# Kernel tuning notes

Measured on AMD Instinct MI355X. Metric: run time of the kernel, lower is better.

The kernel has to match this reference:

```python
import jax, jax.numpy as jnp
import numpy as np


def _gcn_conv(x, W, b, src, dst, n_nodes):
    # PyG GCNConv with add_self_loops=True, edge_weight=None (implicit ones),
    # symmetric normalization: D^{-1/2} A_hat D^{-1/2} (X W) + b
    xw = x @ W                                    # [N, H]
    loop = jnp.arange(n_nodes, dtype=src.dtype)
    src_f = jnp.concatenate([src, loop])          # [E+N]
    dst_f = jnp.concatenate([dst, loop])          # [E+N]
    w = jnp.ones(src_f.shape[0], dtype=x.dtype)
    deg = jax.ops.segment_sum(w, dst_f, num_segments=n_nodes)  # in-degree incl. self-loop
    dinv = jnp.where(deg > 0, jax.lax.rsqrt(deg), 0.0)
    norm = dinv[src_f] * dinv[dst_f]              # [E+N]
    msgs = norm[:, None] * xw[src_f]              # [E+N, H]
    out = jax.ops.segment_sum(msgs, dst_f, num_segments=n_nodes)
    return out + b


def setup_inputs() -> dict:
    key = jax.random.key(0)
    k1, k2, k3, k4 = jax.random.split(key, 4)
    N, E, D, H = 100000, 1600000, 256, 128
    x = jax.random.normal(k1, (N, D), dtype=jnp.float32)
    edge_index = jax.random.randint(k2, (2, E), 0, N, dtype=jnp.int64)
    # Glorot-scaled weights
    W1 = jax.random.normal(k3, (D, H), dtype=jnp.float32) * np.sqrt(2.0 / (D + H))
    b1 = jnp.zeros((H,), dtype=jnp.float32)
    W2 = jax.random.normal(k4, (H, 1), dtype=jnp.float32) * np.sqrt(2.0 / (H + 1))
    b2 = jnp.zeros((1,), dtype=jnp.float32)
    return {"x": x, "edge_index": edge_index, "W1": W1, "b1": b1, "W2": W2, "b2": b2}


def reference(x, edge_index, W1, b1, W2, b2):
    n_nodes = x.shape[0]
    src, dst = edge_index[0], edge_index[1]
    h = _gcn_conv(x, W1, b1, src, dst, n_nodes)   # conv1
    h = jax.nn.relu(h)                            # relu; dropout is identity in eval mode
    out = _gcn_conv(h, W2, b2, src, dst, n_nodes) # conv2 -> [N, 1]
    return out.reshape(-1)                        # x.view(-1)
```

## Files before the change

kernel.cpp:

```cpp
#include <hip/hip_runtime.h>
#include <hip/hip_fp16.h>
#include <cstdint>
#include <cstddef>


#define BSH 9
#define BNODES (1 << BSH)
#define BPAD 16
#define BCAP 9216

typedef _Float16 half8 __attribute__((ext_vector_type(8)));
typedef float floatx4 __attribute__((ext_vector_type(4)));
typedef float floatv4 __attribute__((ext_vector_type(4)));
typedef int intv4 __attribute__((ext_vector_type(4)));
typedef unsigned int uintv4 __attribute__((ext_vector_type(4)));
typedef unsigned int uintv2 __attribute__((ext_vector_type(2)));

#define QK 0x64646464u
#define SEL01 0x00050004u
#define SEL23 0x00070006u

__device__ __forceinline__ void fmamix8(float (&acc)[8], uintv4 v, float w) {
  asm("v_fma_mix_f32 %0, %1, %2, %0 op_sel:[0,0,0] op_sel_hi:[0,1,0]"
      : "+v"(acc[0]) : "v"(w), "v"(v.x));
  asm("v_fma_mix_f32 %0, %1, %2, %0 op_sel:[0,1,0] op_sel_hi:[0,1,0]"
      : "+v"(acc[1]) : "v"(w), "v"(v.x));
  asm("v_fma_mix_f32 %0, %1, %2, %0 op_sel:[0,0,0] op_sel_hi:[0,1,0]"
      : "+v"(acc[2]) : "v"(w), "v"(v.y));
  asm("v_fma_mix_f32 %0, %1, %2, %0 op_sel:[0,1,0] op_sel_hi:[0,1,0]"
      : "+v"(acc[3]) : "v"(w), "v"(v.y));
  asm("v_fma_mix_f32 %0, %1, %2, %0 op_sel:[0,0,0] op_sel_hi:[0,1,0]"
      : "+v"(acc[4]) : "v"(w), "v"(v.z));
  asm("v_fma_mix_f32 %0, %1, %2, %0 op_sel:[0,1,0] op_sel_hi:[0,1,0]"
      : "+v"(acc[5]) : "v"(w), "v"(v.z));
  asm("v_fma_mix_f32 %0, %1, %2, %0 op_sel:[0,0,0] op_sel_hi:[0,1,0]"
      : "+v"(acc[6]) : "v"(w), "v"(v.w));
  asm("v_fma_mix_f32 %0, %1, %2, %0 op_sel:[0,1,0] op_sel_hi:[0,1,0]"
      : "+v"(acc[7]) : "v"(w), "v"(v.w));
}

__device__ __forceinline__ void fmaq8(float (&acc)[8], uintv2 q, float w) {
  uintv4 hw;
  hw.x = __builtin_amdgcn_perm(q.x, QK, SEL01);
  hw.y = __builtin_amdgcn_perm(q.x, QK, SEL23);
  hw.z = __builtin_amdgcn_perm(q.y, QK, SEL01);
  hw.w = __builtin_amdgcn_perm(q.y, QK, SEL23);
  fmamix8(acc, hw, w);
}

#define SWZF(v, imm) \
  __int_as_float(__builtin_amdgcn_ds_swizzle(__float_as_int(v), imm))

__global__ __launch_bounds__(256) void prep_k(const float* __restrict__ W1,
                                              _Float16* __restrict__ wz,
                                              unsigned char* __restrict__ z1q8,
                                              float* __restrict__ scp,
                                              float* __restrict__ z2w,
                                              int* __restrict__ cnt,
                                              int* __restrict__ gcur,
                                              int N, int NB) {
  int b = blockIdx.x, tid = threadIdx.x;
  if (b < 128) {
    int id = b * 256 + tid;
    int j = id & 7, lane = (id >> 3) & 63, nb = (id >> 9) & 7, kb = id >> 12;
    int k = kb * 32 + ((lane >> 4) << 3) + j;
    int n = nb * 16 + (lane & 15);
    wz[id] = (_Float16)W1[k * 128 + n];
  } else if (b == 128) {
    if (tid < 32) ((unsigned*)(z1q8 + (size_t)N * 128))[tid] = 0x80808080u;
    if (tid == 0) { z2w[N] = 0.f; cnt[N] = 1; scp[N] = 1.f; }
  } else {
    int i = (b - 129) * 256 + tid;
    if (i < NB * BPAD) gcur[i] = 0;
  }
}

template <int KIND>
__global__ __launch_bounds__(256) void stage_k(int fb, int g0,
                                               const float* __restrict__ X,
                                               const _Float16* __restrict__ wz,
                                               unsigned char* __restrict__ z1q8,
                                               float* __restrict__ scp, int N,
                                               const int* __restrict__ src,
                                               const int* __restrict__ dst,
                                               int* __restrict__ gcur,
                                               int* __restrict__ barr,
                                               int* __restrict__ ell,
                                               int* __restrict__ ell2,
                                               int* __restrict__ cnt,
                                               int E, int NB) {
  __shared__ char lds_raw[16 * 1024 + 256];
  int tid = threadIdx.x;

  if ((int)blockIdx.x < fb) {
    if (KIND == 0) {
      int* bc = (int*)lds_raw;
      int* bb = bc + 512;
      for (int i = tid; i < NB; i += 256) bc[i] = 0;
      __syncthreads();
      int base = ((int)blockIdx.x * 256 + tid) * 16;
      int dv[16], sv[16], rv[16], bkv[16];
      int ne = 0;
      if (base + 15 < E) {
#pragma unroll
        for (int q4 = 0; q4 < 4; ++q4) {
          intv4 d4 = __builtin_nontemporal_load((const intv4*)(dst + base + q4 * 4));
          intv4 s4 = __builtin_nontemporal_load((const intv4*)(src + base + q4 * 4));
          dv[q4 * 4 + 0] = d4[0]; dv[q4 * 4 + 1] = d4[1];
          dv[q4 * 4 + 2] = d4[2]; dv[q4 * 4 + 3] = d4[3];
          sv[q4 * 4 + 0] = s4[0]; sv[q4 * 4 + 1] = s4[1];
          sv[q4 * 4 + 2] = s4[2]; sv[q4 * 4 + 3] = s4[3];
        }
        ne = 16;
      } else {
        for (int e = base; e < E && e < base + 16; ++e) {
          dv[ne] = dst[e]; sv[ne] = src[e]; ++ne;
        }
      }
      for (int i = 0; i < ne; ++i) {
        bkv[i] = dv[i] >> BSH;
        rv[i] = atomicAdd(&bc[bkv[i]], 1);
      }
      __syncthreads();
      for (int i = tid; i < NB; i += 256) {
        int cc = bc[i];
        bb[i] = cc ? atomicAdd(&gcur[i * BPAD], cc) : 0;
      }
      __syncthreads();
      for (int i = 0; i < ne; ++i) {
        int pos = bb[bkv[i]] + rv[i];
        if (pos < BCAP) {
          unsigned dl = (unsigned)(dv[i] & (BNODES - 1));
          barr[(size_t)bkv[i] * BCAP + pos] = (int)((dl << 23) | (unsigned)sv[i]);
        }
      }
    } else {
      int* cl = (int*)lds_raw;
      int bkt = (int)blockIdx.x;
      int lo = bkt << BSH;
      for (int i = tid; i < BNODES; i += 256) {
        cl[i] = 1;
        int node = lo + i;
        if (node < N) ell[(size_t)node * 32] = node;
      }
      __syncthreads();
      int cb = min(gcur[bkt * BPAD], BCAP);
      const int* seg = barr + (size_t)bkt * BCAP;
      for (int e = tid; e < cb; e += 256) {
        unsigned v = (unsigned)seg[e];
        int dl = (int)(v >> 23);
        int s = (int)(v & 0x7FFFFFu);
        int p = atomicAdd(&cl[dl], 1);
        if (p < 32) ell[(size_t)(lo + dl) * 32 + p] = s;
        else if (p < 63) ell2[(size_t)(lo + dl) * 32 + (p - 32)] = s;
      }
      __syncthreads();
      for (int i = tid; i < BNODES; i += 256) {
        int node = lo + i;
        if (node < N) cnt[node] = cl[i];
      }
    }
    return;
  }

  _Float16* Bl = (_Float16*)lds_raw;
  _Float16* Ol = (_Float16*)lds_raw;
  float* invl = (float*)(lds_raw + 16 * 1024);

  int wave = tid >> 6, lane = tid & 63;
  int m = lane & 15, q = lane >> 4;
  int row0 = (g0 + (int)blockIdx.x - fb) * 64;
  int row = row0 + wave * 16 + m;

  floatx4 acc[8];
#pragma unroll
  for (int nb = 0; nb < 8; ++nb) acc[nb] = (floatx4)(0.f);

  const uintv4* wsrc = (const uintv4*)wz;
  uintv4* bdst = (uintv4*)Bl;

#pragma unroll
  for (int ph = 0; ph < 4; ++ph) {
    if (ph) __syncthreads();
#pragma unroll
    for (int i = 0; i < 4; ++i) bdst[i * 256 + tid] = wsrc[ph * 1024 + i * 256 + tid];
    __syncthreads();
#pragma unroll
    for (int kk = 0; kk < 2; ++kk) {
      int kb = ph * 2 + kk;
      half8 a;
      if (row < N) {
        const floatv4* ap = (const floatv4*)(X + (size_t)row * 256 + kb * 32 + q * 8);
        floatv4 a0 = __builtin_nontemporal_load(ap);
        floatv4 a1 = __builtin_nontemporal_load(ap + 1);
        a[0] = (_Float16)a0[0]; a[1] = (_Float16)a0[1];
        a[2] = (_Float16)a0[2]; a[3] = (_Float16)a0[3];
        a[4] = (_Float16)a1[0]; a[5] = (_Float16)a1[1];
        a[6] = (_Float16)a1[2]; a[7] = (_Float16)a1[3];
      } else {
#pragma unroll
        for (int j = 0; j < 8; ++j) a[j] = (_Float16)0.f;
      }
#pragma unroll
      for (int nb = 0; nb < 8; ++nb) {
        half8 b = *(const half8*)(Bl + ((size_t)(kk * 8 + nb) * 64 + lane) * 8);
        acc[nb] = __builtin_amdgcn_mfma_f32_16x16x32_f16(a, b, acc[nb], 0, 0, 0);
      }
    }
  }

  float rmax[4];
#pragma unroll
  for (int r = 0; r < 4; ++r) rmax[r] = 1e-6f;
#pragma unroll
  for (int nb = 0; nb < 8; ++nb)
#pragma unroll
    for (int r = 0; r < 4; ++r) rmax[r] = fmaxf(rmax[r], fabsf(acc[nb][r]));
#pragma unroll
  for (int r = 0; r < 4; ++r) {
    float v = rmax[r];
    v = fmaxf(v, __shfl_xor(v, 1, 64));
    v = fmaxf(v, __shfl_xor(v, 2, 64));
    v = fmaxf(v, __shfl_xor(v, 4, 64));
    v = fmaxf(v, __shfl_xor(v, 8, 64));
    rmax[r] = v;
  }
  __syncthreads();

#pragma unroll
  for (int nb = 0; nb < 8; ++nb) {
    int col = nb * 16 + m;
#pragma unroll
    for (int r = 0; r < 4; ++r) {
      int orow = wave * 16 + q * 4 + r;
      Ol[orow * 128 + col] = (_Float16)acc[nb][r];
    }
  }
  if (m == 0) {
#pragma unroll
    for (int r = 0; r < 4; ++r) {
      int tr = wave * 16 + q * 4 + r;
      float inv = 126.5f / rmax[r];
      invl[tr] = inv;
      int rw = row0 + tr;
      if (rw < N) scp[rw] = rmax[r] * (1.f / 126.5f);
    }
  }
  __syncthreads();

  const uintv4* osrc = (const uintv4*)Ol;
#pragma unroll
  for (int i = 0; i < 4; ++i) {
    int idx = i * 256 + tid;
    int r = idx >> 4;
    int fb8 = idx & 15;
    if (row0 + r < N) {
      uintv4 v = osrc[idx];
      half8 hv = __builtin_bit_cast(half8, v);
      float inv = invl[r];
      unsigned bq[8];
#pragma unroll
      for (int j = 0; j < 8; ++j) {
        float t = fmaf((float)hv[j], inv, 1152.0f);
        _Float16 ht = (_Float16)t;
        bq[j] = (unsigned)__builtin_bit_cast(unsigned short, ht) & 0xFFu;
      }
      uintv2 o;
      o.x = bq[0] | (bq[1] << 8) | (bq[2] << 16) | (bq[3] << 24);
      o.y = bq[4] | (bq[5] << 8) | (bq[6] << 16) | (bq[7] << 24);
      *(uintv2*)(z1q8 + (size_t)(row0 + r) * 128 + fb8 * 8) = o;
    }
  }
}

__global__ __launch_bounds__(256) void agg1_k(const unsigned char* __restrict__ z1q8,
                                              const float* __restrict__ scp,
                                              const int* __restrict__ cnt,
                                              const int* __restrict__ ell,
                                              const int* __restrict__ ell2,
                                              const float* __restrict__ b1,
                                              const float* __restrict__ W2,
                                              float* __restrict__ z2w, int N) {
  int d = blockIdx.x * 4 + (threadIdx.x >> 6);
  int lane = threadIdx.x & 63;
  if (d >= N) return;
  int cntd = cnt[d];
  int ct = min(cntd, 63);
  int raw;
  if (ct > 32) {
    raw = (lane < 32) ? ell[(size_t)d * 32 + lane]
                      : (lane < 63 ? ell2[(size_t)d * 32 + (lane - 32)] : N);
  } else {
    raw = ell[(size_t)d * 32 + (lane & 31)];
  }
  int idx = (lane < ct) ? raw : N;
  float ws = rsqrtf((float)cnt[idx]) * scp[idx];
  float dd = rsqrtf((float)cntd);
  int iw = __float_as_int(ws);

  int g = lane >> 4;
  unsigned a8 = (unsigned)(lane & 15) << 3;
  const unsigned char* zb = z1q8;
  int pa = g << 2;
  int ax = (lane ^ 32) << 2;

  float acc[8] = {0.f, 0.f, 0.f, 0.f, 0.f, 0.f, 0.f, 0.f};
  float bs = 0.f;

  int t = 0;
  for (; t + 16 <= ct; t += 16) {
    int a0 = pa + (t << 2);
    int s0 = __builtin_amdgcn_ds_bpermute(a0, idx);
    int s1 = __builtin_amdgcn_ds_bpermute(a0 + 16, idx);
    int s2 = __builtin_amdgcn_ds_bpermute(a0 + 32, idx);
    int s3 = __builtin_amdgcn_ds_bpermute(a0 + 48, idx);
    float w0 = __int_as_float(__builtin_amdgcn_ds_bpermute(a0, iw));
    float w1 = __int_as_float(__builtin_amdgcn_ds_bpermute(a0 + 16, iw));
    float w2 = __int_as_float(__builtin_amdgcn_ds_bpermute(a0 + 32, iw));
    float w3 = __int_as_float(__builtin_amdgcn_ds_bpermute(a0 + 48, iw));
    uintv2 q0 = *(const uintv2*)(zb + (((unsigned)s0) << 7) + a8);
    uintv2 q1 = *(const uintv2*)(zb + (((unsigned)s1) << 7) + a8);
    uintv2 q2 = *(const uintv2*)(zb + (((unsigned)s2) << 7) + a8);
    uintv2 q3 = *(const uintv2*)(zb + (((unsigned)s3) << 7) + a8);
    fmaq8(acc, q0, w0);
    fmaq8(acc, q1, w1);
    fmaq8(acc, q2, w2);
    fmaq8(acc, q3, w3);
    bs += (w0 + w1) + (w2 + w3);
  }
  for (; t < ct; t += 4) {
    int a0 = pa + (t << 2);
    int s0 = __builtin_amdgcn_ds_bpermute(a0, idx);
    float w0 = __int_as_float(__builtin_amdgcn_ds_bpermute(a0, iw));
    uintv2 q0 = *(const uintv2*)(zb + (((unsigned)s0) << 7) + a8);
    fmaq8(acc, q0, w0);
    bs += w0;
  }

#pragma unroll
  for (int k = 0; k < 8; ++k) {
    float x = acc[k];
    x += SWZF(x, 0x401F);
    x += __int_as_float(__builtin_amdgcn_ds_bpermute(ax, __float_as_int(x)));
    acc[k] = x;
  }
  bs += SWZF(bs, 0x401F);
  bs += __int_as_float(__builtin_amdgcn_ds_bpermute(ax, __float_as_int(bs)));
  float corr = 1152.f * bs;

  int a8f = (lane & 15) * 8;
  float4 bA = *(const float4*)(b1 + a8f);
  float4 bB = *(const float4*)(b1 + a8f + 4);
  float4 wA = *(const float4*)(W2 + a8f);
  float4 wB = *(const float4*)(W2 + a8f + 4);
  float dot = fmaxf(fmaf(dd, acc[0] - corr, bA.x), 0.f) * wA.x
            + fmaxf(fmaf(dd, acc[1] - corr, bA.y), 0.f) * wA.y
            + fmaxf(fmaf(dd, acc[2] - corr, bA.z), 0.f) * wA.z
            + fmaxf(fmaf(dd, acc[3] - corr, bA.w), 0.f) * wA.w
            + fmaxf(fmaf(dd, acc[4] - corr, bB.x), 0.f) * wB.x
            + fmaxf(fmaf(dd, acc[5] - corr, bB.y), 0.f) * wB.y
            + fmaxf(fmaf(dd, acc[6] - corr, bB.z), 0.f) * wB.z
            + fmaxf(fmaf(dd, acc[7] - corr, bB.w), 0.f) * wB.w;
  dot += SWZF(dot, 0x201F);
  dot += SWZF(dot, 0x101F);
  dot += SWZF(dot, 0x081F);
  dot += SWZF(dot, 0x041F);
  if (lane == 0) z2w[d] = dd * dot;
}

__global__ __launch_bounds__(256) void agg2_k(const float* __restrict__ z2w,
                                              const int* __restrict__ cnt,
                                              const int* __restrict__ ell,
                                              const int* __restrict__ ell2,
                                              const float* __restrict__ b2,
                                              float* __restrict__ out, int N) {
  int wv = threadIdx.x >> 6;
  int half = (threadIdx.x >> 5) & 1;
  int j = threadIdx.x & 31;
  int d = blockIdx.x * 8 + wv * 2 + half;
  if (d >= N) return;
  int cd = cnt[d];
  int c = min(cd, 63);
  int raw = ell[(size_t)d * 32 + j];
  int idx = (j < min(c, 32)) ? raw : N;
  float v = z2w[idx];
  if (c > 32 && j < c - 32) v += z2w[ell2[(size_t)d * 32 + j]];
#pragma unroll
  for (int off = 16; off >= 1; off >>= 1) v += __shfl_xor(v, off, 64);
  if (j == 0) out[d] = rsqrtf((float)cd) * v + b2[0];
}

extern "C" void kernel_launch(void* const* d_in, const int* in_sizes, int n_in,
                              void* d_out, int out_size, void* d_ws, size_t ws_size,
                              hipStream_t stream) {
  (void)n_in; (void)out_size; (void)ws_size;
  const float* x = (const float*)d_in[0];
  const int* edge = (const int*)d_in[1];
  const float* W1 = (const float*)d_in[2];
  const float* b1 = (const float*)d_in[3];
  const float* W2 = (const float*)d_in[4];
  const float* b2 = (const float*)d_in[5];
  float* out = (float*)d_out;

  const int D = 256, H = 128;
  int N = in_sizes[0] / D;
  int E = in_sizes[1] / 2;
  const int* srcp = edge;
  const int* dstp = edge + E;
  int NB = (N + BNODES - 1) >> BSH;

  char* ws = (char*)d_ws;
  size_t off = 0;
  auto alloc = [&](size_t bytes) -> void* {
    void* p = ws + off;
    off += (bytes + 255) & ~(size_t)255;
    return p;
  };
  int* cnt            = (int*)alloc((size_t)(N + 1) * 4);
  float* z2w          = (float*)alloc((size_t)(N + 1) * 4);
  float* scp          = (float*)alloc((size_t)(N + 1) * 4);
  int* ell            = (int*)alloc((size_t)N * 32 * 4);
  int* ell2           = (int*)alloc((size_t)N * 32 * 4);
  _Float16* wz        = (_Float16*)alloc((size_t)32768 * 2);
  unsigned char* z1q8 = (unsigned char*)alloc((size_t)(N + 1) * 128);
  int* gcur           = (int*)alloc((size_t)NB * BPAD * 4);
  int* barr           = (int*)alloc((size_t)NB * BCAP * 4);

  int tiles = (N + 63) / 64;
  int fbA = (E + 4095) / 4096;
  int fbB = NB;

  int T2 = tiles / 2;
  int T1 = tiles - T2;

  prep_k<<<dim3(129 + (NB * BPAD + 255) / 256), dim3(256), 0, stream>>>(
      W1, wz, z1q8, scp, z2w, cnt, gcur, N, NB);
  stage_k<0><<<dim3(fbA + T1), dim3(256), 0, stream>>>(fbA, 0, x, wz, z1q8, scp,
      N, srcp, dstp, gcur, barr, ell, ell2, cnt, E, NB);
  stage_k<1><<<dim3(fbB + T2), dim3(256), 0, stream>>>(fbB, T1, x, wz, z1q8, scp,
      N, srcp, dstp, gcur, barr, ell, ell2, cnt, E, NB);
  agg1_k<<<dim3((N + 3) / 4), dim3(256), 0, stream>>>(z1q8, scp, cnt, ell, ell2,
      b1, W2, z2w, N);
  agg2_k<<<dim3((N + 7) / 8), dim3(256), 0, stream>>>(z2w, cnt, ell, ell2, b2, out, N);
}
```

Before: 272.0 us.

## Pack per-edge source weights into ELL entries and widen agg1 gathers to 16 bytes

Degree counting moves into the edge-bucketing pass through global atomics, so the bucket-fill pass can precompute each source's normalized weight (rsqrt(deg)*scale) and store it beside the source index as 64-bit ELL entries. The aggregation kernel then reads the weight directly instead of doing dependent gathers of cnt and scp per neighbor. It also processes 8 neighbors per wave step with 16-byte quantized-row loads instead of 16 neighbors with 8-byte loads. All GEMM tiles now run in the first stage launch. The trade-offs are doubled ELL storage and traffic (agg2 reads 8-byte entries but uses only the index), plus many global atomics on cnt.

```diff
diff --git a/kernel.cpp b/kernel.cpp
--- a/kernel.cpp
+++ b/kernel.cpp
@@ -20,7 +20,7 @@
 #define SEL01 0x00050004u
 #define SEL23 0x00070006u
 
-__device__ __forceinline__ void fmamix8(float (&acc)[8], uintv4 v, float w) {
+__device__ __forceinline__ void fmamix8(float* acc, uintv4 v, float w) {
   asm("v_fma_mix_f32 %0, %1, %2, %0 op_sel:[0,0,0] op_sel_hi:[0,1,0]"
       : "+v"(acc[0]) : "v"(w), "v"(v.x));
   asm("v_fma_mix_f32 %0, %1, %2, %0 op_sel:[0,1,0] op_sel_hi:[0,1,0]"
@@ -39,13 +39,18 @@
       : "+v"(acc[7]) : "v"(w), "v"(v.w));
 }
 
-__device__ __forceinline__ void fmaq8(float (&acc)[8], uintv2 q, float w) {
-  uintv4 hw;
-  hw.x = __builtin_amdgcn_perm(q.x, QK, SEL01);
-  hw.y = __builtin_amdgcn_perm(q.x, QK, SEL23);
-  hw.z = __builtin_amdgcn_perm(q.y, QK, SEL01);
-  hw.w = __builtin_amdgcn_perm(q.y, QK, SEL23);
-  fmamix8(acc, hw, w);
+__device__ __forceinline__ void fmaq16(float (&acc)[16], uintv4 q, float w) {
+  uintv4 hwA, hwB;
+  hwA.x = __builtin_amdgcn_perm(q.x, QK, SEL01);
+  hwA.y = __builtin_amdgcn_perm(q.x, QK, SEL23);
+  hwA.z = __builtin_amdgcn_perm(q.y, QK, SEL01);
+  hwA.w = __builtin_amdgcn_perm(q.y, QK, SEL23);
+  hwB.x = __builtin_amdgcn_perm(q.z, QK, SEL01);
+  hwB.y = __builtin_amdgcn_perm(q.z, QK, SEL23);
+  hwB.z = __builtin_amdgcn_perm(q.w, QK, SEL01);
+  hwB.w = __builtin_amdgcn_perm(q.w, QK, SEL23);
+  fmamix8(&acc[0], hwA, w);
+  fmamix8(&acc[8], hwB, w);
 }
 
 #define SWZF(v, imm) \
@@ -54,7 +59,6 @@
 __global__ __launch_bounds__(256) void prep_k(const float* __restrict__ W1,
                                               _Float16* __restrict__ wz,
                                               unsigned char* __restrict__ z1q8,
-                                              float* __restrict__ scp,
                                               float* __restrict__ z2w,
                                               int* __restrict__ cnt,
                                               int* __restrict__ gcur,
@@ -68,10 +72,16 @@
     wz[id] = (_Float16)W1[k * 128 + n];
   } else if (b == 128) {
     if (tid < 32) ((unsigned*)(z1q8 + (size_t)N * 128))[tid] = 0x80808080u;
-    if (tid == 0) { z2w[N] = 0.f; cnt[N] = 1; scp[N] = 1.f; }
+    if (tid == 0) z2w[N] = 0.f;
   } else {
-    int i = (b - 129) * 256 + tid;
-    if (i < NB * BPAD) gcur[i] = 0;
+    int CB = (N + 256) / 256;
+    if (b < 129 + CB) {
+      int i = (b - 129) * 256 + tid;
+      if (i <= N) cnt[i] = 1;
+    } else {
+      int i = (b - 129 - CB) * 256 + tid;
+      if (i < NB * BPAD) gcur[i] = 0;
+    }
   }
 }
 
@@ -85,8 +95,8 @@
                                                const int* __restrict__ dst,
                                                int* __restrict__ gcur,
                                                int* __restrict__ barr,
-                                               int* __restrict__ ell,
-                                               int* __restrict__ ell2,
+                                               uintv2* __restrict__ ell64,
+                                               uintv2* __restrict__ ell2_64,
                                                int* __restrict__ cnt,
                                                int E, int NB) {
   __shared__ char lds_raw[16 * 1024 + 256];
@@ -120,6 +130,7 @@
       for (int i = 0; i < ne; ++i) {
         bkv[i] = dv[i] >> BSH;
         rv[i] = atomicAdd(&bc[bkv[i]], 1);
+        atomicAdd(&cnt[dv[i]], 1);
       }
       __syncthreads();
       for (int i = tid; i < NB; i += 256) {
@@ -141,7 +152,12 @@
       for (int i = tid; i < BNODES; i += 256) {
         cl[i] = 1;
         int node = lo + i;
-        if (node < N) ell[(size_t)node * 32] = node;
+        if (node < N) {
+          uintv2 en;
+          en.x = (unsigned)node;
+          en.y = (unsigned)__float_as_int(rsqrtf((float)cnt[node]) * scp[node]);
+          ell64[(size_t)node * 32] = en;
+        }
       }
       __syncthreads();
       int cb = min(gcur[bkt * BPAD], BCAP);
@@ -150,14 +166,13 @@
         unsigned v = (unsigned)seg[e];
         int dl = (int)(v >> 23);
         int s = (int)(v & 0x7FFFFFu);
+        float wsf = rsqrtf((float)cnt[s]) * scp[s];
         int p = atomicAdd(&cl[dl], 1);
-        if (p < 32) ell[(size_t)(lo + dl) * 32 + p] = s;
-        else if (p < 63) ell2[(size_t)(lo + dl) * 32 + (p - 32)] = s;
-      }
-      __syncthreads();
-      for (int i = tid; i < BNODES; i += 256) {
-        int node = lo + i;
-        if (node < N) cnt[node] = cl[i];
+        uintv2 en;
+        en.x = (unsigned)s;
+        en.y = (unsigned)__float_as_int(wsf);
+        if (p < 32) ell64[(size_t)(lo + dl) * 32 + p] = en;
+        else if (p < 63) ell2_64[(size_t)(lo + dl) * 32 + (p - 32)] = en;
       }
     }
     return;
@@ -274,10 +289,9 @@
 }
 
 __global__ __launch_bounds__(256) void agg1_k(const unsigned char* __restrict__ z1q8,
-                                              const float* __restrict__ scp,
                                               const int* __restrict__ cnt,
-                                              const int* __restrict__ ell,
-                                              const int* __restrict__ ell2,
+                                              const uintv2* __restrict__ ell64,
+                                              const uintv2* __restrict__ ell2_64,
                                               const float* __restrict__ b1,
                                               const float* __restrict__ W2,
                                               float* __restrict__ z2w, int N) {
@@ -286,92 +300,81 @@
   if (d >= N) return;
   int cntd = cnt[d];
   int ct = min(cntd, 63);
-  int raw;
+  uintv2 en;
+  en.x = (unsigned)N; en.y = 0x3F800000u;
   if (ct > 32) {
-    raw = (lane < 32) ? ell[(size_t)d * 32 + lane]
-                      : (lane < 63 ? ell2[(size_t)d * 32 + (lane - 32)] : N);
+    if (lane < 32)      en = ell64[(size_t)d * 32 + lane];
+    else if (lane < 63) en = ell2_64[(size_t)d * 32 + (lane - 32)];
   } else {
-    raw = ell[(size_t)d * 32 + (lane & 31)];
-  }
-  int idx = (lane < ct) ? raw : N;
-  float ws = rsqrtf((float)cnt[idx]) * scp[idx];
+    en = ell64[(size_t)d * 32 + (lane & 31)];
+  }
+  int idx = (lane < ct) ? (int)en.x : N;
+  float ws = (lane < ct) ? __int_as_float((int)en.y) : 1.0f;
   float dd = rsqrtf((float)cntd);
   int iw = __float_as_int(ws);
 
-  int g = lane >> 4;
-  unsigned a8 = (unsigned)(lane & 15) << 3;
+  int g = lane >> 3;
+  unsigned a16 = (unsigned)(lane & 7) << 4;
   const unsigned char* zb = z1q8;
-  int pa = g << 2;
   int ax = (lane ^ 32) << 2;
 
-  float acc[8] = {0.f, 0.f, 0.f, 0.f, 0.f, 0.f, 0.f, 0.f};
+  float acc[16];
+#pragma unroll
+  for (int k = 0; k < 16; ++k) acc[k] = 0.f;
   float bs = 0.f;
 
   int t = 0;
   for (; t + 16 <= ct; t += 16) {
-    int a0 = pa + (t << 2);
+    int a0 = (t + g) << 2;
     int s0 = __builtin_amdgcn_ds_bpermute(a0, idx);
-    int s1 = __builtin_amdgcn_ds_bpermute(a0 + 16, idx);
-    int s2 = __builtin_amdgcn_ds_bpermute(a0 + 32, idx);
-    int s3 = __builtin_amdgcn_ds_bpermute(a0 + 48, idx);
+    int s1 = __builtin_amdgcn_ds_bpermute(a0 + 32, idx);
     float w0 = __int_as_float(__builtin_amdgcn_ds_bpermute(a0, iw));
-    float w1 = __int_as_float(__builtin_amdgcn_ds_bpermute(a0 + 16, iw));
-    float w2 = __int_as_float(__builtin_amdgcn_ds_bpermute(a0 + 32, iw));
-    float w3 = __int_as_float(__builtin_amdgcn_ds_bpermute(a0 + 48, iw));
-    uintv2 q0 = *(const uintv2*)(zb + (((unsigned)s0) << 7) + a8);
-    uintv2 q1 = *(const uintv2*)(zb + (((unsigned)s1) << 7) + a8);
-    uintv2 q2 = *(const uintv2*)(zb + (((unsigned)s2) << 7) + a8);
-    uintv2 q3 = *(const uintv2*)(zb + (((unsigned)s3) << 7) + a8);
-    fmaq8(acc, q0, w0);
-    fmaq8(acc, q1, w1);
-    fmaq8(acc, q2, w2);
-    fmaq8(acc, q3, w3);
-    bs += (w0 + w1) + (w2 + w3);
-  }
-  for (; t < ct; t += 4) {
-    int a0 = pa + (t << 2);
+    float w1 = __int_as_float(__builtin_amdgcn_ds_bpermute(a0 + 32, iw));
+    uintv4 q0 = *(const uintv4*)(zb + (((unsigned)s0) << 7) + a16);
+    uintv4 q1 = *(const uintv4*)(zb + (((unsigned)s1) << 7) + a16);
+    fmaq16(acc, q0, w0);
+    fmaq16(acc, q1, w1);
+    bs += w0 + w1;
+  }
+  for (; t < ct; t += 8) {
+    int a0 = (t + g) << 2;
     int s0 = __builtin_amdgcn_ds_bpermute(a0, idx);
     float w0 = __int_as_float(__builtin_amdgcn_ds_bpermute(a0, iw));
-    uintv2 q0 = *(const uintv2*)(zb + (((unsigned)s0) << 7) + a8);
-    fmaq8(acc, q0, w0);
+    uintv4 q0 = *(const uintv4*)(zb + (((unsigned)s0) << 7) + a16);
+    fmaq16(acc, q0, w0);
     bs += w0;
   }
 
 #pragma unroll
-  for (int k = 0; k < 8; ++k) {
+  for (int k = 0; k < 16; ++k) {
     float x = acc[k];
+    x += SWZF(x, 0x201F);
     x += SWZF(x, 0x401F);
     x += __int_as_float(__builtin_amdgcn_ds_bpermute(ax, __float_as_int(x)));
     acc[k] = x;
   }
+  bs += SWZF(bs, 0x201F);
   bs += SWZF(bs, 0x401F);
   bs += __int_as_float(__builtin_amdgcn_ds_bpermute(ax, __float_as_int(bs)));
   float corr = 1152.f * bs;
 
-  int a8f = (lane & 15) * 8;
-  float4 bA = *(const float4*)(b1 + a8f);
-  float4 bB = *(const float4*)(b1 + a8f + 4);
-  float4 wA = *(const float4*)(W2 + a8f);
-  float4 wB = *(const float4*)(W2 + a8f + 4);
-  float dot = fmaxf(fmaf(dd, acc[0] - corr, bA.x), 0.f) * wA.x
-            + fmaxf(fmaf(dd, acc[1] - corr, bA.y), 0.f) * wA.y
-            + fmaxf(fmaf(dd, acc[2] - corr, bA.z), 0.f) * wA.z
-            + fmaxf(fmaf(dd, acc[3] - corr, bA.w), 0.f) * wA.w
-            + fmaxf(fmaf(dd, acc[4] - corr, bB.x), 0.f) * wB.x
-            + fmaxf(fmaf(dd, acc[5] - corr, bB.y), 0.f) * wB.y
-            + fmaxf(fmaf(dd, acc[6] - corr, bB.z), 0.f) * wB.z
-            + fmaxf(fmaf(dd, acc[7] - corr, bB.w), 0.f) * wB.w;
-  dot += SWZF(dot, 0x201F);
+  int fb = (lane & 7) * 16;
+  const float* bp = b1 + fb;
+  const float* wp = W2 + fb;
+  float dot = 0.f;
+#pragma unroll
+  for (int k = 0; k < 16; ++k)
+    dot += fmaxf(fmaf(dd, acc[k] - corr, bp[k]), 0.f) * wp[k];
+  dot += SWZF(dot, 0x041F);
+  dot += SWZF(dot, 0x081F);
   dot += SWZF(dot, 0x101F);
-  dot += SWZF(dot, 0x081F);
-  dot += SWZF(dot, 0x041F);
   if (lane == 0) z2w[d] = dd * dot;
 }
 
 __global__ __launch_bounds__(256) void agg2_k(const float* __restrict__ z2w,
                                               const int* __restrict__ cnt,
-                                              const int* __restrict__ ell,
-                                              const int* __restrict__ ell2,
+                                              const uintv2* __restrict__ ell64,
+                                              const uintv2* __restrict__ ell2_64,
                                               const float* __restrict__ b2,
                                               float* __restrict__ out, int N) {
   int wv = threadIdx.x >> 6;
@@ -381,10 +384,10 @@
   if (d >= N) return;
   int cd = cnt[d];
   int c = min(cd, 63);
-  int raw = ell[(size_t)d * 32 + j];
-  int idx = (j < min(c, 32)) ? raw : N;
+  uintv2 e = ell64[(size_t)d * 32 + j];
+  int idx = (j < min(c, 32)) ? (int)e.x : N;
   float v = z2w[idx];
-  if (c > 32 && j < c - 32) v += z2w[ell2[(size_t)d * 32 + j]];
+  if (c > 32 && j < c - 32) v += z2w[(int)ell2_64[(size_t)d * 32 + j].x];
 #pragma unroll
   for (int off = 16; off >= 1; off >>= 1) v += __shfl_xor(v, off, 64);
   if (j == 0) out[d] = rsqrtf((float)cd) * v + b2[0];
@@ -419,8 +422,8 @@
   int* cnt            = (int*)alloc((size_t)(N + 1) * 4);
   float* z2w          = (float*)alloc((size_t)(N + 1) * 4);
   float* scp          = (float*)alloc((size_t)(N + 1) * 4);
-  int* ell            = (int*)alloc((size_t)N * 32 * 4);
-  int* ell2           = (int*)alloc((size_t)N * 32 * 4);
+  uintv2* ell64       = (uintv2*)alloc((size_t)N * 32 * 8);
+  uintv2* ell2_64     = (uintv2*)alloc((size_t)N * 32 * 8);
   _Float16* wz        = (_Float16*)alloc((size_t)32768 * 2);
   unsigned char* z1q8 = (unsigned char*)alloc((size_t)(N + 1) * 128);
   int* gcur           = (int*)alloc((size_t)NB * BPAD * 4);
@@ -429,17 +432,16 @@
   int tiles = (N + 63) / 64;
   int fbA = (E + 4095) / 4096;
   int fbB = NB;
-
-  int T2 = tiles / 2;
-  int T1 = tiles - T2;
-
-  prep_k<<<dim3(129 + (NB * BPAD + 255) / 256), dim3(256), 0, stream>>>(
-      W1, wz, z1q8, scp, z2w, cnt, gcur, N, NB);
-  stage_k<0><<<dim3(fbA + T1), dim3(256), 0, stream>>>(fbA, 0, x, wz, z1q8, scp,
-      N, srcp, dstp, gcur, barr, ell, ell2, cnt, E, NB);
-  stage_k<1><<<dim3(fbB + T2), dim3(256), 0, stream>>>(fbB, T1, x, wz, z1q8, scp,
-      N, srcp, dstp, gcur, barr, ell, ell2, cnt, E, NB);
-  agg1_k<<<dim3((N + 3) / 4), dim3(256), 0, stream>>>(z1q8, scp, cnt, ell, ell2,
+  int CB = (N + 256) / 256;
+
+  prep_k<<<dim3(129 + CB + (NB * BPAD + 255) / 256), dim3(256), 0, stream>>>(
+      W1, wz, z1q8, z2w, cnt, gcur, N, NB);
+  stage_k<0><<<dim3(fbA + tiles), dim3(256), 0, stream>>>(fbA, 0, x, wz, z1q8,
+      scp, N, srcp, dstp, gcur, barr, ell64, ell2_64, cnt, E, NB);
+  stage_k<1><<<dim3(fbB), dim3(256), 0, stream>>>(fbB, tiles, x, wz, z1q8,
+      scp, N, srcp, dstp, gcur, barr, ell64, ell2_64, cnt, E, NB);
+  agg1_k<<<dim3((N + 3) / 4), dim3(256), 0, stream>>>(z1q8, cnt, ell64, ell2_64,
       b1, W2, z2w, N);
-  agg2_k<<<dim3((N + 7) / 8), dim3(256), 0, stream>>>(z2w, cnt, ell, ell2, b2, out, N);
-}
+  agg2_k<<<dim3((N + 7) / 8), dim3(256), 0, stream>>>(z2w, cnt, ell64, ell2_64,
+      b2, out, N);
+}
```

Result: slower. 343.4 us (+26.2%).

## Precompute per-node source weights and move all GEMM tiles into first stage

Applied to the files above, without the earlier changes.

Moves the entire X·W1 GEMM tile work into the first stage launch, which runs alongside edge bucketing, so that the second stage only builds the ELL lists. This lets the second stage read the per-row scale (scp) for every node and write a combined weight rsqrt(deg)*scp into a new wst array. agg1 then does one gathered load per neighbor instead of two (cnt and scp) plus an rsqrt. The trade-off is that the first launch now carries all GEMM tiles, which can unbalance how work overlaps across the two stage launches.

```diff
diff --git a/kernel.cpp b/kernel.cpp
--- a/kernel.cpp
+++ b/kernel.cpp
@@ -20,7 +20,7 @@
 #define SEL01 0x00050004u
 #define SEL23 0x00070006u
 
-__device__ __forceinline__ void fmamix8(float (&acc)[8], uintv4 v, float w) {
+__device__ __forceinline__ void fmamix8(float* acc, uintv4 v, float w) {
   asm("v_fma_mix_f32 %0, %1, %2, %0 op_sel:[0,0,0] op_sel_hi:[0,1,0]"
       : "+v"(acc[0]) : "v"(w), "v"(v.x));
   asm("v_fma_mix_f32 %0, %1, %2, %0 op_sel:[0,1,0] op_sel_hi:[0,1,0]"
@@ -54,7 +54,7 @@
 __global__ __launch_bounds__(256) void prep_k(const float* __restrict__ W1,
                                               _Float16* __restrict__ wz,
                                               unsigned char* __restrict__ z1q8,
-                                              float* __restrict__ scp,
+                                              float* __restrict__ wst,
                                               float* __restrict__ z2w,
                                               int* __restrict__ cnt,
                                               int* __restrict__ gcur,
@@ -68,7 +68,7 @@
     wz[id] = (_Float16)W1[k * 128 + n];
   } else if (b == 128) {
     if (tid < 32) ((unsigned*)(z1q8 + (size_t)N * 128))[tid] = 0x80808080u;
-    if (tid == 0) { z2w[N] = 0.f; cnt[N] = 1; scp[N] = 1.f; }
+    if (tid == 0) { z2w[N] = 0.f; cnt[N] = 1; wst[N] = 1.f; }
   } else {
     int i = (b - 129) * 256 + tid;
     if (i < NB * BPAD) gcur[i] = 0;
@@ -80,7 +80,8 @@
                                                const float* __restrict__ X,
                                                const _Float16* __restrict__ wz,
                                                unsigned char* __restrict__ z1q8,
-                                               float* __restrict__ scp, int N,
+                                               float* __restrict__ scp,
+                                               float* __restrict__ wst, int N,
                                                const int* __restrict__ src,
                                                const int* __restrict__ dst,
                                                int* __restrict__ gcur,
@@ -157,7 +158,11 @@
       __syncthreads();
       for (int i = tid; i < BNODES; i += 256) {
         int node = lo + i;
-        if (node < N) cnt[node] = cl[i];
+        if (node < N) {
+          int c = cl[i];
+          cnt[node] = c;
+          wst[node] = rsqrtf((float)c) * scp[node];
+        }
       }
     }
     return;
@@ -274,7 +279,7 @@
 }
 
 __global__ __launch_bounds__(256) void agg1_k(const unsigned char* __restrict__ z1q8,
-                                              const float* __restrict__ scp,
+                                              const float* __restrict__ wst,
                                               const int* __restrict__ cnt,
                                               const int* __restrict__ ell,
                                               const int* __restrict__ ell2,
@@ -294,7 +299,7 @@
     raw = ell[(size_t)d * 32 + (lane & 31)];
   }
   int idx = (lane < ct) ? raw : N;
-  float ws = rsqrtf((float)cnt[idx]) * scp[idx];
+  float ws = (lane < ct) ? wst[idx] : 1.0f;
   float dd = rsqrtf((float)cntd);
   int iw = __float_as_int(ws);
 
@@ -419,6 +424,7 @@
   int* cnt            = (int*)alloc((size_t)(N + 1) * 4);
   float* z2w          = (float*)alloc((size_t)(N + 1) * 4);
   float* scp          = (float*)alloc((size_t)(N + 1) * 4);
+  float* wst          = (float*)alloc((size_t)(N + 1) * 4);
   int* ell            = (int*)alloc((size_t)N * 32 * 4);
   int* ell2           = (int*)alloc((size_t)N * 32 * 4);
   _Float16* wz        = (_Float16*)alloc((size_t)32768 * 2);
@@ -430,16 +436,13 @@
   int fbA = (E + 4095) / 4096;
   int fbB = NB;
 
-  int T2 = tiles / 2;
-  int T1 = tiles - T2;
-
   prep_k<<<dim3(129 + (NB * BPAD + 255) / 256), dim3(256), 0, stream>>>(
-      W1, wz, z1q8, scp, z2w, cnt, gcur, N, NB);
-  stage_k<0><<<dim3(fbA + T1), dim3(256), 0, stream>>>(fbA, 0, x, wz, z1q8, scp,
-      N, srcp, dstp, gcur, barr, ell, ell2, cnt, E, NB);
-  stage_k<1><<<dim3(fbB + T2), dim3(256), 0, stream>>>(fbB, T1, x, wz, z1q8, scp,
-      N, srcp, dstp, gcur, barr, ell, ell2, cnt, E, NB);
-  agg1_k<<<dim3((N + 3) / 4), dim3(256), 0, stream>>>(z1q8, scp, cnt, ell, ell2,
+      W1, wz, z1q8, wst, z2w, cnt, gcur, N, NB);
+  stage_k<0><<<dim3(fbA + tiles), dim3(256), 0, stream>>>(fbA, 0, x, wz, z1q8,
+      scp, wst, N, srcp, dstp, gcur, barr, ell, ell2, cnt, E, NB);
+  stage_k<1><<<dim3(fbB), dim3(256), 0, stream>>>(fbB, tiles, x, wz, z1q8,
+      scp, wst, N, srcp, dstp, gcur, barr, ell, ell2, cnt, E, NB);
+  agg1_k<<<dim3((N + 3) / 4), dim3(256), 0, stream>>>(z1q8, wst, cnt, ell, ell2,
       b1, W2, z2w, N);
   agg2_k<<<dim3((N + 7) / 8), dim3(256), 0, stream>>>(z2w, cnt, ell, ell2, b2, out, N);
 }
```

Result: faster. 266.5 us (-2.0%).
